# Optimization experiments

Hardware: AMD Instinct MI355X
Metric: run time of the kernel (lower is better)

The kernel has to match this reference:

```python
import jax, jax.numpy as jnp
import numpy as np

B, C, V, L = 64, 32, 1024, 12
ORDER = 2


def setup_inputs() -> dict:
    key = jax.random.key(0)
    ks = jax.random.split(key, 6)
    x = jax.random.normal(ks[0], (B, C, V, L), dtype=jnp.float32)
    A1 = jax.random.uniform(ks[1], (V, V), dtype=jnp.float32)
    A2 = jax.random.uniform(ks[2], (V, V), dtype=jnp.float32)
    nodevec1 = jax.random.normal(ks[3], (V, 10), dtype=jnp.float32)
    nodevec2 = jax.random.normal(ks[4], (10, V), dtype=jnp.float32)
    c_cat = (ORDER * 3 + 1) * C  # 7*C = 224, matches gcn: (order*support_len+1)*c_in
    W_mlp = jax.random.normal(ks[5], (C, c_cat), dtype=jnp.float32) * 0.05
    b_mlp = jnp.zeros((C,), dtype=jnp.float32)
    return {"x": x, "A1": A1, "A2": A2, "nodevec1": nodevec1,
            "nodevec2": nodevec2, "W_mlp": W_mlp, "b_mlp": b_mlp}


def reference(x, A1, A2, nodevec1, nodevec2, W_mlp, b_mlp):
    # adaptive adjacency: softmax(relu(E1 @ E2), dim=1)  (graph-wavenet style)
    adp = jax.nn.softmax(jax.nn.relu(nodevec1 @ nodevec2), axis=1)  # [V, V]
    supports = (A1, A2, adp)
    # gcn.forward: multi-hop diffusion via nconv einsum, order=2
    out = [x]
    for a in supports:
        x1 = jnp.einsum('ncvl,vw->ncwl', x, a)   # hop 1
        out.append(x1)
        x2 = jnp.einsum('ncvl,vw->ncwl', x1, a)  # hop 2
        out.append(x2)
    h = jnp.concatenate(out, axis=1)             # [B, 7C, V, L]
    # linear: 1x1 Conv2d over channel dim (dropout is identity in eval)
    h = jnp.einsum('ncvl,oc->novl', h, W_mlp) + b_mlp[None, :, None, None]
    return h
```

## Files before the change

### kernel.cpp

```cpp
#include <hip/hip_runtime.h>
#include <hip/hip_bf16.h>


typedef __attribute__((ext_vector_type(8))) short short8;
typedef __attribute__((ext_vector_type(4))) float floatx4;

#define V_DIM 1024
#define L_DIM 12
#define B_DIM 64
#define C_DIM 32

__global__ __launch_bounds__(128) void adp_kernel(
    const float* __restrict__ nv1, const float* __restrict__ nv2,
    float* __restrict__ adp) {
  const int v = blockIdx.x, tid = threadIdx.x;
  float n1[10];
#pragma unroll
  for (int i = 0; i < 10; ++i) n1[i] = nv1[v * 10 + i];
  __shared__ float red[128];
  float e[8];
  float lmax = -1e30f;
#pragma unroll
  for (int j = 0; j < 8; ++j) {
    int w = tid + j * 128;
    float s = 0.f;
#pragma unroll
    for (int i = 0; i < 10; ++i) s += n1[i] * nv2[i * V_DIM + w];
    s = fmaxf(s, 0.f);
    e[j] = s;
    lmax = fmaxf(lmax, s);
  }
  red[tid] = lmax; __syncthreads();
  for (int s = 64; s > 0; s >>= 1) {
    if (tid < s) red[tid] = fmaxf(red[tid], red[tid + s]);
    __syncthreads();
  }
  float mx = red[0]; __syncthreads();
  float lsum = 0.f;
#pragma unroll
  for (int j = 0; j < 8; ++j) { e[j] = __expf(e[j] - mx); lsum += e[j]; }
  red[tid] = lsum; __syncthreads();
  for (int s = 64; s > 0; s >>= 1) {
    if (tid < s) red[tid] += red[tid + s];
    __syncthreads();
  }
  float inv = 1.f / red[0];
#pragma unroll
  for (int j = 0; j < 8; ++j) adp[(size_t)v * V_DIM + tid + j * 128] = e[j] * inv;
}

__global__ __launch_bounds__(256) void cast_transpose(
    const float* __restrict__ A1, const float* __restrict__ A2,
    const float* __restrict__ adp, __hip_bfloat16* __restrict__ As,
    __hip_bfloat16* __restrict__ BtCat) {
  const int z = blockIdx.z;
  const float* src = (z == 0) ? A1 : (z == 1) ? A2 : adp;
  __hip_bfloat16* sdst = As + (size_t)z * V_DIM * V_DIM;
  __hip_bfloat16* tdst = BtCat + (size_t)(2 * z) * V_DIM * V_DIM;
  __shared__ float tile[64][65];
  const int v0 = blockIdx.y * 64, w0 = blockIdx.x * 64;
  const int tc = threadIdx.x & 15, tr = threadIdx.x >> 4;
#pragma unroll
  for (int i = 0; i < 4; ++i) {
    int r = tr + i * 16;
    float4 val = *(const float4*)(src + (size_t)(v0 + r) * V_DIM + w0 + tc * 4);
    tile[r][tc * 4 + 0] = val.x; tile[r][tc * 4 + 1] = val.y;
    tile[r][tc * 4 + 2] = val.z; tile[r][tc * 4 + 3] = val.w;
    __hip_bfloat16* sp = sdst + (size_t)(v0 + r) * V_DIM + w0 + tc * 4;
    sp[0] = __float2bfloat16(val.x); sp[1] = __float2bfloat16(val.y);
    sp[2] = __float2bfloat16(val.z); sp[3] = __float2bfloat16(val.w);
  }
  __syncthreads();
#pragma unroll
  for (int i = 0; i < 4; ++i) {
    int r = tr + i * 16;
    __hip_bfloat16* tp = tdst + (size_t)(w0 + r) * V_DIM + v0 + tc * 4;
#pragma unroll
    for (int j = 0; j < 4; ++j) tp[j] = __float2bfloat16(tile[tc * 4 + j][r]);
  }
}

__global__ __launch_bounds__(256) void transpose_x_k(
    const float* __restrict__ x, __hip_bfloat16* __restrict__ xT) {
  const int bc = blockIdx.x;
  const int b = bc >> 5, c = bc & 31;
  __shared__ __align__(16) __hip_bfloat16 tile[V_DIM * L_DIM];
  const float4* src = (const float4*)(x + (size_t)bc * (V_DIM * L_DIM));
#pragma unroll
  for (int i = 0; i < 12; ++i) {
    int idx = threadIdx.x + i * 256;
    float4 v = src[idx];
    int e = idx * 4;
    tile[e + 0] = __float2bfloat16(v.x); tile[e + 1] = __float2bfloat16(v.y);
    tile[e + 2] = __float2bfloat16(v.z); tile[e + 3] = __float2bfloat16(v.w);
  }
  __syncthreads();
  for (int l = 0; l < L_DIM; ++l) {
    __hip_bfloat16* dst = xT + ((size_t)(b * L_DIM + l) * C_DIM + c) * V_DIM;
    for (int v = threadIdx.x; v < V_DIM; v += 256) dst[v] = tile[v * L_DIM + l];
  }
}

__device__ __forceinline__ void gll16(const __hip_bfloat16* g, __hip_bfloat16* l) {
  __builtin_amdgcn_global_load_lds(
      (const __attribute__((address_space(1))) void*)g,
      (__attribute__((address_space(3))) void*)l, 16, 0, 0);
}

template <int MODE>
__global__ __launch_bounds__(256) void gemm_bt(
    const __hip_bfloat16* __restrict__ Abase,
    const __hip_bfloat16* __restrict__ Btbase,
    __hip_bfloat16* __restrict__ Cbase, int M, int N, int K,
    long long aStride, long long bStride, long long cStride) {
  const __hip_bfloat16* A = Abase + (size_t)blockIdx.z * aStride;
  const __hip_bfloat16* Bt = Btbase + (size_t)blockIdx.z * bStride;
  __hip_bfloat16* C = Cbase + (size_t)blockIdx.z * cStride;
  __shared__ __align__(16) __hip_bfloat16 lA[128 * 64];
  __shared__ __align__(16) __hip_bfloat16 lB[128 * 64];
  const int tid = threadIdx.x;
  const int wv = tid >> 6, lane = tid & 63;
  const int wm = wv >> 1, wn = wv & 1;
  const int m0 = blockIdx.y * 128, n0 = blockIdx.x * 128;
  const int lrow = lane >> 3, lcol = lane & 7;
  const int gcol = lcol ^ (lrow & 7);
  const int fr = lane & 15, quad = lane >> 4;
  const int sw = fr & 7;

  floatx4 acc[4][4];
#pragma unroll
  for (int i = 0; i < 4; ++i)
#pragma unroll
    for (int j = 0; j < 4; ++j) acc[i][j] = (floatx4){0.f, 0.f, 0.f, 0.f};

  for (int kt = 0; kt < K; kt += 64) {
    __syncthreads();
#pragma unroll
    for (int i = 0; i < 4; ++i) {
      int r0 = (wv * 4 + i) * 8;
      gll16(A + (size_t)(m0 + r0 + lrow) * K + kt + gcol * 8, &lA[r0 * 64]);
      gll16(Bt + (size_t)(n0 + r0 + lrow) * K + kt + gcol * 8, &lB[r0 * 64]);
    }
    __syncthreads();
#pragma unroll
    for (int ks = 0; ks < 2; ++ks) {
      const int chunk = (ks * 4 + quad) ^ sw;
      short8 af[4], bfr[4];
#pragma unroll
      for (int t = 0; t < 4; ++t) {
        af[t] = *(const short8*)&lA[(wm * 64 + t * 16 + fr) * 64 + chunk * 8];
        bfr[t] = *(const short8*)&lB[(wn * 64 + t * 16 + fr) * 64 + chunk * 8];
      }
#pragma unroll
      for (int i = 0; i < 4; ++i)
#pragma unroll
        for (int j = 0; j < 4; ++j)
          acc[i][j] = __builtin_amdgcn_mfma_f32_16x16x32_bf16(af[i], bfr[j], acc[i][j], 0, 0, 0);
    }
  }
#pragma unroll
  for (int i = 0; i < 4; ++i) {
#pragma unroll
    for (int j = 0; j < 4; ++j) {
      int mb = m0 + wm * 64 + i * 16 + quad * 4;
      int n = n0 + wn * 64 + j * 16 + fr;
#pragma unroll
      for (int r = 0; r < 4; ++r) {
        int m = mb + r;
        float val = acc[i][j][r];
        size_t idx;
        if (MODE == 0) {
          idx = (size_t)m * N + n;
        } else {
          int c = m & 31, bl = m >> 5, k = n >> 10, w = n & 1023;
          idx = (((size_t)bl * 6 + k) * 32 + c) * 1024 + w;
        }
        C[idx] = __float2bfloat16(val);
      }
    }
  }
}

__global__ __launch_bounds__(256) void mix_kernel(
    const __hip_bfloat16* __restrict__ R, const __hip_bfloat16* __restrict__ xT,
    const float* __restrict__ W, const float* __restrict__ bias,
    float* __restrict__ out) {
  const int b = blockIdx.y, wt = blockIdx.x;
  const int tid = threadIdx.x;
  __shared__ __align__(16) __hip_bfloat16 tile[L_DIM * C_DIM * 64];
  __shared__ float Wl[7 * 32 * 32];
  for (int i = tid; i < 7168; i += 256) {
    int o = i / 224, cc = i - o * 224;
    Wl[cc * 32 + o] = W[i];
  }
  float acc[3][32];
#pragma unroll
  for (int pt = 0; pt < 3; ++pt)
#pragma unroll
    for (int o = 0; o < 32; ++o) acc[pt][o] = bias[o];
  int wloc[3], ll[3];
#pragma unroll
  for (int pt = 0; pt < 3; ++pt) {
    int wl = tid + pt * 256;
    wloc[pt] = wl / 12;
    ll[pt] = wl - wloc[pt] * 12;
  }
  const int w0 = wt * 64;
  for (int k = 0; k < 7; ++k) {
    __syncthreads();
    const __hip_bfloat16* srcp = (k < 6) ? R : xT;
    const int rps = (k < 6) ? 192 : 32;
    const int ko = (k < 6) ? k * 32 : 0;
#pragma unroll
    for (int i = 0; i < 24; ++i) {
      int q = tid + i * 256;
      int rr = q >> 4, ci = q & 15;
      int l = rr >> 5, c = rr & 31;
      size_t rowg = (size_t)(b * L_DIM + l) * rps + ko + c;
      *(ushort4*)&tile[rr * 64 + ci * 4] =
          *(const ushort4*)&srcp[rowg * V_DIM + w0 + ci * 4];
    }
    __syncthreads();
    const float* Wp = &Wl[((k < 6) ? (k + 1) : 0) * 1024];
    const int base0 = ll[0] * 2048 + wloc[0];
    const int base1 = ll[1] * 2048 + wloc[1];
    const int base2 = ll[2] * 2048 + wloc[2];
#pragma unroll 8
    for (int c = 0; c < 32; ++c) {
      float v0 = __bfloat162float(tile[base0 + c * 64]);
      float v1 = __bfloat162float(tile[base1 + c * 64]);
      float v2 = __bfloat162float(tile[base2 + c * 64]);
#pragma unroll
      for (int o = 0; o < 32; ++o) {
        float wv = Wp[c * 32 + o];
        acc[0][o] += wv * v0;
        acc[1][o] += wv * v1;
        acc[2][o] += wv * v2;
      }
    }
  }
  const size_t obase = (size_t)b * (32 * V_DIM * L_DIM) + (size_t)w0 * L_DIM;
#pragma unroll
  for (int o = 0; o < 32; ++o) {
    size_t base = obase + (size_t)o * (V_DIM * L_DIM);
    out[base + tid] = acc[0][o];
    out[base + tid + 256] = acc[1][o];
    out[base + tid + 512] = acc[2][o];
  }
}

extern "C" void kernel_launch(void* const* d_in, const int* in_sizes, int n_in,
                              void* d_out, int out_size, void* d_ws,
                              size_t ws_size, hipStream_t stream) {
  const float* x = (const float*)d_in[0];
  const float* A1 = (const float*)d_in[1];
  const float* A2 = (const float*)d_in[2];
  const float* nv1 = (const float*)d_in[3];
  const float* nv2 = (const float*)d_in[4];
  const float* W = (const float*)d_in[5];
  const float* bias = (const float*)d_in[6];
  float* out = (float*)d_out;

  char* ws = (char*)d_ws;
  __hip_bfloat16* R = (__hip_bfloat16*)(ws + 0);
  __hip_bfloat16* xT = (__hip_bfloat16*)(ws + 301989888ull);
  __hip_bfloat16* BtCat = (__hip_bfloat16*)(ws + 352321536ull);
  __hip_bfloat16* As = (__hip_bfloat16*)(ws + 364904448ull);
  float* adp = (float*)(ws + 371195904ull);

  adp_kernel<<<dim3(1024), dim3(128), 0, stream>>>(nv1, nv2, adp);
  cast_transpose<<<dim3(16, 16, 3), dim3(256), 0, stream>>>(A1, A2, adp, As, BtCat);
  gemm_bt<0><<<dim3(8, 8, 3), dim3(256), 0, stream>>>(
      BtCat, As, BtCat + 1048576ull, 1024, 1024, 1024,
      2097152ll, 1048576ll, 2097152ll);
  transpose_x_k<<<dim3(2048), dim3(256), 0, stream>>>(x, xT);
  gemm_bt<1><<<dim3(48, 192, 1), dim3(256), 0, stream>>>(
      xT, BtCat, R, 24576, 6144, 1024, 0ll, 0ll, 0ll);
  mix_kernel<<<dim3(16, 64), dim3(256), 0, stream>>>(R, xT, W, bias, out);
}
```

Measured before the change: 797.4 us.

## Apply channel-mixing weights before diffusion and fuse output into concatenated-K GEMM

Uses linearity to apply W_mlp to x first (y_kernel computes seven 32-channel projections), then runs one big GEMM with K=6144 over the concatenated transposed supports, adding the bias and the identity term in the epilogue and writing float output directly. This removes the large intermediate R tensor and the separate mix kernel, and the GEMM N shrinks from 6144 to 1024 while K grows. The supports are now stored in an interleaved [w][6*1024] layout. The output store is strided (stride 12 floats per n), which may be uncoalesced.

```diff
diff --git a/kernel.cpp b/kernel.cpp
--- a/kernel.cpp
+++ b/kernel.cpp
@@ -9,6 +9,7 @@
 #define L_DIM 12
 #define B_DIM 64
 #define C_DIM 32
+#define KCAT 6144
 
 __global__ __launch_bounds__(128) void adp_kernel(
     const float* __restrict__ nv1, const float* __restrict__ nv2,
@@ -52,11 +53,11 @@
 __global__ __launch_bounds__(256) void cast_transpose(
     const float* __restrict__ A1, const float* __restrict__ A2,
     const float* __restrict__ adp, __hip_bfloat16* __restrict__ As,
-    __hip_bfloat16* __restrict__ BtCat) {
+    __hip_bfloat16* __restrict__ BtCat2) {
   const int z = blockIdx.z;
   const float* src = (z == 0) ? A1 : (z == 1) ? A2 : adp;
   __hip_bfloat16* sdst = As + (size_t)z * V_DIM * V_DIM;
-  __hip_bfloat16* tdst = BtCat + (size_t)(2 * z) * V_DIM * V_DIM;
+  __hip_bfloat16* tdst = BtCat2 + (size_t)(2 * z) * V_DIM;
   __shared__ float tile[64][65];
   const int v0 = blockIdx.y * 64, w0 = blockIdx.x * 64;
   const int tc = threadIdx.x & 15, tr = threadIdx.x >> 4;
@@ -74,30 +75,66 @@
 #pragma unroll
   for (int i = 0; i < 4; ++i) {
     int r = tr + i * 16;
-    __hip_bfloat16* tp = tdst + (size_t)(w0 + r) * V_DIM + v0 + tc * 4;
+    __hip_bfloat16* tp = tdst + (size_t)(w0 + r) * KCAT + v0 + tc * 4;
 #pragma unroll
     for (int j = 0; j < 4; ++j) tp[j] = __float2bfloat16(tile[tc * 4 + j][r]);
   }
 }
 
-__global__ __launch_bounds__(256) void transpose_x_k(
-    const float* __restrict__ x, __hip_bfloat16* __restrict__ xT) {
-  const int bc = blockIdx.x;
-  const int b = bc >> 5, c = bc & 31;
-  __shared__ __align__(16) __hip_bfloat16 tile[V_DIM * L_DIM];
-  const float4* src = (const float4*)(x + (size_t)bc * (V_DIM * L_DIM));
-#pragma unroll
-  for (int i = 0; i < 12; ++i) {
-    int idx = threadIdx.x + i * 256;
-    float4 v = src[idx];
-    int e = idx * 4;
-    tile[e + 0] = __float2bfloat16(v.x); tile[e + 1] = __float2bfloat16(v.y);
-    tile[e + 2] = __float2bfloat16(v.z); tile[e + 3] = __float2bfloat16(v.w);
+__global__ __launch_bounds__(256, 3) void y_kernel(
+    const float* __restrict__ x, const float* __restrict__ W,
+    __hip_bfloat16* __restrict__ Ycat, __hip_bfloat16* __restrict__ Y0) {
+  const int b = blockIdx.y, v0 = blockIdx.x * 64;
+  const int tid = threadIdx.x;
+  const int lane = tid & 63;
+  const int wq = __builtin_amdgcn_readfirstlane(tid >> 6);
+  __shared__ __hip_bfloat16 xs[768 * 33];
+#pragma unroll
+  for (int it = 0; it < 24; ++it) {
+    int i = tid + it * 256;
+    int c = i / 192, j = i - c * 192;
+    float4 val = *(const float4*)(x + (size_t)(b * 32 + c) * 12288 + v0 * 12 + j * 4);
+    int e = j * 4;
+    float vv[4] = {val.x, val.y, val.z, val.w};
+#pragma unroll
+    for (int q = 0; q < 4; ++q) {
+      int ee = e + q, v = ee / 12, l = ee - v * 12;
+      xs[(l * 64 + v) * 33 + c] = __float2bfloat16(vv[q]);
+    }
   }
   __syncthreads();
-  for (int l = 0; l < L_DIM; ++l) {
-    __hip_bfloat16* dst = xT + ((size_t)(b * L_DIM + l) * C_DIM + c) * V_DIM;
-    for (int v = threadIdx.x; v < V_DIM; v += 256) dst[v] = tile[v * L_DIM + l];
+  for (int lp = 0; lp < 6; ++lp) {
+    const int l = lp * 2;
+    float xa[32], xb[32];
+#pragma unroll
+    for (int c = 0; c < 32; ++c) {
+      xa[c] = __bfloat162float(xs[(l * 64 + lane) * 33 + c]);
+      xb[c] = __bfloat162float(xs[((l + 1) * 64 + lane) * 33 + c]);
+    }
+    for (int oi = 0; oi < 8; ++oi) {
+      const int o = wq * 8 + oi;
+      const float* Wr = W + o * 224;
+      float aacc[7], bacc[7];
+#pragma unroll
+      for (int kk = 0; kk < 7; ++kk) { aacc[kk] = 0.f; bacc[kk] = 0.f; }
+#pragma unroll
+      for (int c = 0; c < 32; ++c) {
+#pragma unroll
+        for (int kk = 0; kk < 7; ++kk) {
+          float wv = Wr[kk * 32 + c];
+          aacc[kk] += wv * xa[c];
+          bacc[kk] += wv * xb[c];
+        }
+      }
+      const size_t row = (size_t)b * 384 + o * 12 + l;
+      Y0[row * V_DIM + v0 + lane] = __float2bfloat16(aacc[0]);
+      Y0[(row + 1) * V_DIM + v0 + lane] = __float2bfloat16(bacc[0]);
+#pragma unroll
+      for (int kk = 1; kk < 7; ++kk) {
+        Ycat[row * KCAT + (kk - 1) * V_DIM + v0 + lane] = __float2bfloat16(aacc[kk]);
+        Ycat[(row + 1) * KCAT + (kk - 1) * V_DIM + v0 + lane] = __float2bfloat16(bacc[kk]);
+      }
+    }
   }
 }
 
@@ -108,10 +145,12 @@
 }
 
 template <int MODE>
-__global__ __launch_bounds__(256) void gemm_bt(
+__global__ __launch_bounds__(256) void gemm_k(
     const __hip_bfloat16* __restrict__ Abase,
     const __hip_bfloat16* __restrict__ Btbase,
-    __hip_bfloat16* __restrict__ Cbase, int M, int N, int K,
+    __hip_bfloat16* __restrict__ Cbase, float* __restrict__ outp,
+    const __hip_bfloat16* __restrict__ Y0, const float* __restrict__ bias,
+    int K, int lda, int ldb, int ldc,
     long long aStride, long long bStride, long long cStride) {
   const __hip_bfloat16* A = Abase + (size_t)blockIdx.z * aStride;
   const __hip_bfloat16* Bt = Btbase + (size_t)blockIdx.z * bStride;
@@ -138,8 +177,8 @@
 #pragma unroll
     for (int i = 0; i < 4; ++i) {
       int r0 = (wv * 4 + i) * 8;
-      gll16(A + (size_t)(m0 + r0 + lrow) * K + kt + gcol * 8, &lA[r0 * 64]);
-      gll16(Bt + (size_t)(n0 + r0 + lrow) * K + kt + gcol * 8, &lB[r0 * 64]);
+      gll16(A + (size_t)(m0 + r0 + lrow) * lda + kt + gcol * 8, &lA[r0 * 64]);
+      gll16(Bt + (size_t)(n0 + r0 + lrow) * ldb + kt + gcol * 8, &lB[r0 * 64]);
     }
     __syncthreads();
 #pragma unroll
@@ -160,92 +199,34 @@
   }
 #pragma unroll
   for (int i = 0; i < 4; ++i) {
+    const int mb = m0 + wm * 64 + i * 16 + quad * 4;
+    int bq = 0, oq = 0, lq = 0;
+    float bs = 0.f;
+    if (MODE == 2) {
+      bq = mb / 384;
+      int olq = mb - bq * 384;
+      oq = olq / 12;
+      lq = olq - oq * 12;
+      bs = bias[oq];
+    }
 #pragma unroll
     for (int j = 0; j < 4; ++j) {
-      int mb = m0 + wm * 64 + i * 16 + quad * 4;
-      int n = n0 + wn * 64 + j * 16 + fr;
-#pragma unroll
-      for (int r = 0; r < 4; ++r) {
-        int m = mb + r;
-        float val = acc[i][j][r];
-        size_t idx;
-        if (MODE == 0) {
-          idx = (size_t)m * N + n;
-        } else {
-          int c = m & 31, bl = m >> 5, k = n >> 10, w = n & 1023;
-          idx = (((size_t)bl * 6 + k) * 32 + c) * 1024 + w;
-        }
-        C[idx] = __float2bfloat16(val);
-      }
-    }
-  }
-}
-
-__global__ __launch_bounds__(256) void mix_kernel(
-    const __hip_bfloat16* __restrict__ R, const __hip_bfloat16* __restrict__ xT,
-    const float* __restrict__ W, const float* __restrict__ bias,
-    float* __restrict__ out) {
-  const int b = blockIdx.y, wt = blockIdx.x;
-  const int tid = threadIdx.x;
-  __shared__ __align__(16) __hip_bfloat16 tile[L_DIM * C_DIM * 64];
-  __shared__ float Wl[7 * 32 * 32];
-  for (int i = tid; i < 7168; i += 256) {
-    int o = i / 224, cc = i - o * 224;
-    Wl[cc * 32 + o] = W[i];
-  }
-  float acc[3][32];
-#pragma unroll
-  for (int pt = 0; pt < 3; ++pt)
-#pragma unroll
-    for (int o = 0; o < 32; ++o) acc[pt][o] = bias[o];
-  int wloc[3], ll[3];
-#pragma unroll
-  for (int pt = 0; pt < 3; ++pt) {
-    int wl = tid + pt * 256;
-    wloc[pt] = wl / 12;
-    ll[pt] = wl - wloc[pt] * 12;
-  }
-  const int w0 = wt * 64;
-  for (int k = 0; k < 7; ++k) {
-    __syncthreads();
-    const __hip_bfloat16* srcp = (k < 6) ? R : xT;
-    const int rps = (k < 6) ? 192 : 32;
-    const int ko = (k < 6) ? k * 32 : 0;
-#pragma unroll
-    for (int i = 0; i < 24; ++i) {
-      int q = tid + i * 256;
-      int rr = q >> 4, ci = q & 15;
-      int l = rr >> 5, c = rr & 31;
-      size_t rowg = (size_t)(b * L_DIM + l) * rps + ko + c;
-      *(ushort4*)&tile[rr * 64 + ci * 4] =
-          *(const ushort4*)&srcp[rowg * V_DIM + w0 + ci * 4];
-    }
-    __syncthreads();
-    const float* Wp = &Wl[((k < 6) ? (k + 1) : 0) * 1024];
-    const int base0 = ll[0] * 2048 + wloc[0];
-    const int base1 = ll[1] * 2048 + wloc[1];
-    const int base2 = ll[2] * 2048 + wloc[2];
-#pragma unroll 8
-    for (int c = 0; c < 32; ++c) {
-      float v0 = __bfloat162float(tile[base0 + c * 64]);
-      float v1 = __bfloat162float(tile[base1 + c * 64]);
-      float v2 = __bfloat162float(tile[base2 + c * 64]);
-#pragma unroll
-      for (int o = 0; o < 32; ++o) {
-        float wv = Wp[c * 32 + o];
-        acc[0][o] += wv * v0;
-        acc[1][o] += wv * v1;
-        acc[2][o] += wv * v2;
-      }
-    }
-  }
-  const size_t obase = (size_t)b * (32 * V_DIM * L_DIM) + (size_t)w0 * L_DIM;
-#pragma unroll
-  for (int o = 0; o < 32; ++o) {
-    size_t base = obase + (size_t)o * (V_DIM * L_DIM);
-    out[base + tid] = acc[0][o];
-    out[base + tid + 256] = acc[1][o];
-    out[base + tid + 512] = acc[2][o];
+      const int n = n0 + wn * 64 + j * 16 + fr;
+      if (MODE == 0) {
+#pragma unroll
+        for (int r = 0; r < 4; ++r)
+          C[(size_t)(mb + r) * ldc + n] = __float2bfloat16(acc[i][j][r]);
+      } else {
+        float4 val;
+        float* vp = &val.x;
+#pragma unroll
+        for (int r = 0; r < 4; ++r)
+          vp[r] = acc[i][j][r] + bs +
+                  __bfloat162float(Y0[(size_t)(mb + r) * V_DIM + n]);
+        *(float4*)&outp[(size_t)bq * 393216 + (size_t)oq * 12288 +
+                        (size_t)n * 12 + lq] = val;
+      }
+    }
   }
 }
 
@@ -262,19 +243,19 @@
   float* out = (float*)d_out;
 
   char* ws = (char*)d_ws;
-  __hip_bfloat16* R = (__hip_bfloat16*)(ws + 0);
-  __hip_bfloat16* xT = (__hip_bfloat16*)(ws + 301989888ull);
-  __hip_bfloat16* BtCat = (__hip_bfloat16*)(ws + 352321536ull);
+  __hip_bfloat16* Ycat = (__hip_bfloat16*)(ws + 0);
+  __hip_bfloat16* Y0 = (__hip_bfloat16*)(ws + 301989888ull);
+  __hip_bfloat16* BtCat2 = (__hip_bfloat16*)(ws + 352321536ull);
   __hip_bfloat16* As = (__hip_bfloat16*)(ws + 364904448ull);
   float* adp = (float*)(ws + 371195904ull);
 
   adp_kernel<<<dim3(1024), dim3(128), 0, stream>>>(nv1, nv2, adp);
-  cast_transpose<<<dim3(16, 16, 3), dim3(256), 0, stream>>>(A1, A2, adp, As, BtCat);
-  gemm_bt<0><<<dim3(8, 8, 3), dim3(256), 0, stream>>>(
-      BtCat, As, BtCat + 1048576ull, 1024, 1024, 1024,
-      2097152ll, 1048576ll, 2097152ll);
-  transpose_x_k<<<dim3(2048), dim3(256), 0, stream>>>(x, xT);
-  gemm_bt<1><<<dim3(48, 192, 1), dim3(256), 0, stream>>>(
-      xT, BtCat, R, 24576, 6144, 1024, 0ll, 0ll, 0ll);
-  mix_kernel<<<dim3(16, 64), dim3(256), 0, stream>>>(R, xT, W, bias, out);
-}
+  cast_transpose<<<dim3(16, 16, 3), dim3(256), 0, stream>>>(A1, A2, adp, As, BtCat2);
+  gemm_k<0><<<dim3(8, 8, 3), dim3(256), 0, stream>>>(
+      BtCat2, As, BtCat2 + 1024, nullptr, nullptr, nullptr,
+      1024, KCAT, 1024, KCAT, 2048ll, 1048576ll, 2048ll);
+  y_kernel<<<dim3(16, 64), dim3(256), 0, stream>>>(x, W, Ycat, Y0);
+  gemm_k<2><<<dim3(8, 192), dim3(256), 0, stream>>>(
+      Ycat, BtCat2, nullptr, out, Y0, bias,
+      KCAT, KCAT, KCAT, 0, 0ll, 0ll, 0ll);
+}
```

After: 843.8 us. 5.8% more time.
